# Kernel tuning notes

Measured on AMD Instinct MI355X. Metric: run time of the kernel, lower is better.

Reference implementation:

```python
import jax, jax.numpy as jnp
import numpy as np

N_HEAD, D_MODEL, D_K, D_V = 8, 512, 64, 64
B, LQ, LK = 32, 512, 512
NEG = -1e10
EPS = 1e-5


def setup_inputs() -> dict:
    key = jax.random.key(0)
    ks = jax.random.split(key, 9)
    q = jax.random.normal(ks[0], (B, LQ, D_MODEL), jnp.float32)
    k = jax.random.normal(ks[1], (B, LK, D_MODEL), jnp.float32)
    v = jax.random.normal(ks[2], (B, LK, D_MODEL), jnp.float32)
    mask = jax.random.randint(ks[3], (B, LQ, LK), 0, 2).astype(bool)
    std_qk = np.sqrt(2.0 / (D_MODEL + D_K)).astype(np.float32)
    std_v = np.sqrt(2.0 / (D_MODEL + D_V)).astype(np.float32)
    Wq = jax.random.normal(ks[4], (N_HEAD * D_K, D_MODEL), jnp.float32) * std_qk
    Wk = jax.random.normal(ks[5], (N_HEAD * D_K, D_MODEL), jnp.float32) * std_qk
    Wv = jax.random.normal(ks[6], (N_HEAD * D_V, D_MODEL), jnp.float32) * std_v
    fc_w = jax.random.normal(ks[7], (D_MODEL, N_HEAD * D_V), jnp.float32) * np.sqrt(2.0 / (D_MODEL + N_HEAD * D_V)).astype(np.float32)
    fc_b = jnp.zeros((D_MODEL,), jnp.float32)
    ln_g = jnp.ones((D_MODEL,), jnp.float32)
    ln_b = jnp.zeros((D_MODEL,), jnp.float32)
    return {"q": q, "k": k, "v": v, "mask": mask, "Wq": Wq, "Wk": Wk,
            "Wv": Wv, "fc_w": fc_w, "fc_b": fc_b, "ln_g": ln_g, "ln_b": ln_b}


def reference(q, k, v, mask, Wq, Wk, Wv, fc_w, fc_b, ln_g, ln_b):
    b, lq, _ = q.shape
    lk = k.shape[1]
    # projections (torch Linear: x @ W.T), reshape to [b, h, len, d]
    qh = (q @ Wq.T).reshape(b, lq, N_HEAD, D_K).transpose(0, 2, 1, 3)
    kh = (k @ Wk.T).reshape(b, lk, N_HEAD, D_K).transpose(0, 2, 1, 3)
    vh = (v @ Wv.T).reshape(b, lk, N_HEAD, D_V).transpose(0, 2, 1, 3)
    temperature = jnp.asarray(np.power(D_K, 0.5), qh.dtype)
    scores = jnp.einsum('bhqd,bhkd->bhqk', qh, kh) / temperature
    scores = jnp.where(mask[:, None, :, :], NEG, scores)  # masked_fill
    attn = jax.nn.softmax(scores, axis=-1)  # dropout in eval mode = identity
    out = jnp.einsum('bhqk,bhkd->bhqd', attn, vh)  # [b, h, lq, dv]
    out = out.transpose(0, 2, 1, 3).reshape(b, lq, N_HEAD * D_V)
    out = out @ fc_w.T + fc_b
    # layernorm over last dim
    mu = out.mean(-1, keepdims=True)
    var = ((out - mu) ** 2).mean(-1, keepdims=True)
    out = (out - mu) * jax.lax.rsqrt(var + EPS) * ln_g + ln_b
    # attn returned as [n_head*b, lq, lk] (head-major, matching torch view)
    attn_flat = attn.transpose(1, 0, 2, 3).reshape(N_HEAD * b, lq, lk)
    return out, attn_flat
```

## Files before the change

kernel.cpp:

```cpp
#include <hip/hip_runtime.h>
#include <stdint.h>


typedef float f32x4 __attribute__((ext_vector_type(4)));
typedef __bf16 bf16x8 __attribute__((ext_vector_type(8)));

#define DEV __device__ __forceinline__

DEV uint16_t f2bf(float f) {
  uint32_t u = __builtin_bit_cast(uint32_t, f);
  u += 0x7fffu + ((u >> 16) & 1u);
  return (uint16_t)(u >> 16);
}

DEV void gload_lds16(const void* g, void* l) {
  __builtin_amdgcn_global_load_lds((const __attribute__((address_space(1))) uint32_t*)g,
                                   (__attribute__((address_space(3))) uint32_t*)l, 16, 0, 0);
}

__global__ __launch_bounds__(256) void cvt_bf16(const float* __restrict__ src,
                                                uint16_t* __restrict__ dst, int n4) {
  int i = blockIdx.x * 256 + threadIdx.x;
  if (i >= n4) return;
  f32x4 v = ((const f32x4*)src)[i];
  ushort4 o;
  o.x = f2bf(v.x); o.y = f2bf(v.y); o.z = f2bf(v.z); o.w = f2bf(v.w);
  ((ushort4*)dst)[i] = o;
}

__global__ __launch_bounds__(256) void pack_mask(const int* __restrict__ m,
                                                 unsigned long long* __restrict__ pm, int nw) {
  int t = blockIdx.x * 256 + threadIdx.x;
  int wid = t >> 6, lane = t & 63;
  if (wid >= nw) return;
  int v = m[(size_t)wid * 64 + lane];
  unsigned long long bits = __ballot(v != 0);
  if (lane == 0) pm[wid] = bits;
}

template <int EPI>
__global__ __launch_bounds__(256) void gemm_nt(const uint16_t* __restrict__ A,
                                               const uint16_t* __restrict__ Bw,
                                               void* __restrict__ outp) {
  __shared__ uint16_t As[2][128 * 64];
  __shared__ uint16_t Bs[2][128 * 64];
  const int t = threadIdx.x;
  const int lane = t & 63;
  const int w = t >> 6;
  const int bn = blockIdx.x & 3;
  const int bm = blockIdx.x >> 2;
  const char* Ab = (const char*)(A + (size_t)bm * 128 * 512);
  const char* Bb = (const char*)(Bw + (size_t)bn * 128 * 512);
  const int l15 = lane & 15, l4 = lane >> 4;
  const int wr = (w >> 1) * 64, wc = (w & 1) * 64;

  auto stage = [&](int buf, int kt) {
    const int kb = kt * 128;
#pragma unroll
    for (int i = 0; i < 4; ++i) {
      int o = i * 4096 + t * 16;
      int row = o >> 7, cb = o & 127;
      int sw = cb ^ ((row & 7) << 4);
      gload_lds16(Ab + (size_t)row * 1024 + kb + sw, (char*)As[buf] + i * 4096 + (t & 192) * 16);
      gload_lds16(Bb + (size_t)row * 1024 + kb + sw, (char*)Bs[buf] + i * 4096 + (t & 192) * 16);
    }
  };

  f32x4 acc[4][4] = {};
  stage(0, 0);
  __syncthreads();
#pragma unroll 1
  for (int kt = 0; kt < 8; ++kt) {
    int cur = kt & 1;
    if (kt < 7) stage(cur ^ 1, kt + 1);
#pragma unroll
    for (int kk = 0; kk < 2; ++kk) {
      bf16x8 af[4], bf[4];
#pragma unroll
      for (int i = 0; i < 4; ++i) {
        int ar = wr + i * 16 + l15;
        af[i] = *(const bf16x8*)((const char*)As[cur] + ar * 128 +
                                 ((kk * 64 + l4 * 16) ^ ((ar & 7) << 4)));
        int br = wc + i * 16 + l15;
        bf[i] = *(const bf16x8*)((const char*)Bs[cur] + br * 128 +
                                 ((kk * 64 + l4 * 16) ^ ((br & 7) << 4)));
      }
#pragma unroll
      for (int i = 0; i < 4; ++i)
#pragma unroll
        for (int j = 0; j < 4; ++j)
          acc[i][j] = __builtin_amdgcn_mfma_f32_16x16x32_bf16(af[i], bf[j], acc[i][j], 0, 0, 0);
    }
    __syncthreads();
  }

  const int m0 = bm * 128 + wr + l4 * 4;
  const int n0 = bn * 128 + wc + l15;
#pragma unroll
  for (int i = 0; i < 4; ++i) {
#pragma unroll
    for (int j = 0; j < 4; ++j) {
      int mm = m0 + i * 16;
      int nn = n0 + j * 16;
      if (EPI == 2) {
        float* dst = (float*)outp + (size_t)mm * 512 + nn;
#pragma unroll
        for (int r = 0; r < 4; ++r) dst[(size_t)r * 512] = acc[i][j][r];
      } else {
        int b = mm >> 9, l = mm & 511;
        int h = nn >> 6, d = nn & 63;
        if (EPI == 0) {
          uint16_t* dst = (uint16_t*)outp + ((size_t)(b * 8 + h) * 512 + l) * 64 + d;
#pragma unroll
          for (int r = 0; r < 4; ++r) dst[(size_t)r * 64] = f2bf(acc[i][j][r]);
        } else {
          uint16_t* dst = (uint16_t*)outp + ((size_t)(b * 8 + h) * 64 + d) * 512 + l;
          ushort4 o;
          o.x = f2bf(acc[i][j][0]); o.y = f2bf(acc[i][j][1]);
          o.z = f2bf(acc[i][j][2]); o.w = f2bf(acc[i][j][3]);
          *(ushort4*)dst = o;
        }
      }
    }
  }
}

__global__ __launch_bounds__(512) void attn_fused(const uint16_t* __restrict__ qh,
                                                  const uint16_t* __restrict__ kh,
                                                  const uint16_t* __restrict__ vtp,
                                                  const unsigned long long* __restrict__ pm,
                                                  float* __restrict__ attn_out,
                                                  uint16_t* __restrict__ oh) {
  __shared__ uint16_t Qs[64 * 64];
  __shared__ uint16_t Ks[256 * 64];
  __shared__ uint16_t VTs[64 * 256];
  __shared__ uint16_t Ps[64 * 512];
  __shared__ float red8[64 * 8];
  __shared__ float redF[64];
  __shared__ float redS[64];

  const int bid = blockIdx.x;
  const int qb = bid & 7, h = (bid >> 3) & 7, b = bid >> 6;
  const int t = threadIdx.x, lane = t & 63, w = t >> 6;
  const int l15 = lane & 15, l4 = lane >> 4;
  const int q0 = qb * 64;
  const char* qbase = (const char*)(qh + ((size_t)(b * 8 + h) * 512 + q0) * 64);
  const char* kbase = (const char*)(kh + (size_t)(b * 8 + h) * 512 * 64);
  const char* vbase = (const char*)(vtp + (size_t)(b * 8 + h) * 64 * 512);

  auto stageK = [&](int p) {
#pragma unroll
    for (int i = 0; i < 4; ++i) {
      int o = i * 8192 + t * 16, row = o >> 7, cb = o & 127;
      gload_lds16(kbase + (size_t)(p * 256 + row) * 128 + (cb ^ ((row & 7) << 4)),
                  (char*)Ks + i * 8192 + (t & 448) * 16);
    }
  };
  auto stageV = [&](int p) {
#pragma unroll
    for (int i = 0; i < 4; ++i) {
      int o = i * 8192 + t * 16, row = o >> 9, cb = o & 511;
      gload_lds16(vbase + (size_t)row * 1024 + p * 512 + (cb ^ ((row & 7) << 4)),
                  (char*)VTs + i * 8192 + (t & 448) * 16);
    }
  };
  {
    int o = t * 16, row = o >> 7, cb = o & 127;
    gload_lds16(qbase + (size_t)row * 128 + (cb ^ ((row & 7) << 4)), (char*)Qs + (t & 448) * 16);
  }
  stageK(0);
  stageV(0);
  __syncthreads();

  bf16x8 af[4][2];
#pragma unroll
  for (int fq = 0; fq < 4; ++fq)
#pragma unroll
    for (int kk = 0; kk < 2; ++kk) {
      int ar = fq * 16 + l15;
      af[fq][kk] = *(const bf16x8*)((const char*)Qs + ar * 128 +
                                    ((kk * 64 + l4 * 16) ^ ((ar & 7) << 4)));
    }

  f32x4 sacc[4][4] = {};
#pragma unroll
  for (int fc = 0; fc < 2; ++fc) {
    int brow = w * 32 + fc * 16 + l15;
    bf16x8 b0 = *(const bf16x8*)((const char*)Ks + brow * 128 + ((l4 * 16) ^ ((brow & 7) << 4)));
    bf16x8 b1 = *(const bf16x8*)((const char*)Ks + brow * 128 + ((64 + l4 * 16) ^ ((brow & 7) << 4)));
#pragma unroll
    for (int fq = 0; fq < 4; ++fq) {
      sacc[fq][fc] = __builtin_amdgcn_mfma_f32_16x16x32_bf16(af[fq][0], b0, sacc[fq][fc], 0, 0, 0);
      sacc[fq][fc] = __builtin_amdgcn_mfma_f32_16x16x32_bf16(af[fq][1], b1, sacc[fq][fc], 0, 0, 0);
    }
  }
  __syncthreads();
  stageK(1);
  __syncthreads();
#pragma unroll
  for (int fc = 0; fc < 2; ++fc) {
    int brow = w * 32 + fc * 16 + l15;
    bf16x8 b0 = *(const bf16x8*)((const char*)Ks + brow * 128 + ((l4 * 16) ^ ((brow & 7) << 4)));
    bf16x8 b1 = *(const bf16x8*)((const char*)Ks + brow * 128 + ((64 + l4 * 16) ^ ((brow & 7) << 4)));
#pragma unroll
    for (int fq = 0; fq < 4; ++fq) {
      sacc[fq][2 + fc] = __builtin_amdgcn_mfma_f32_16x16x32_bf16(af[fq][0], b0, sacc[fq][2 + fc], 0, 0, 0);
      sacc[fq][2 + fc] = __builtin_amdgcn_mfma_f32_16x16x32_bf16(af[fq][1], b1, sacc[fq][2 + fc], 0, 0, 0);
    }
  }

  const size_t pmbase = ((size_t)b * 512 + q0) * 8;
#pragma unroll
  for (int fq = 0; fq < 4; ++fq) {
#pragma unroll
    for (int i = 0; i < 4; ++i) {
      int r = fq * 16 + l4 * 4 + i;
      unsigned long long m0 = pm[pmbase + r * 8 + (w >> 1)];
      unsigned long long m1 = pm[pmbase + r * 8 + 4 + (w >> 1)];
      int bit0 = (w & 1) * 32 + l15;
      float vmax = -3.0e38f;
#pragma unroll
      for (int fc = 0; fc < 4; ++fc) {
        unsigned long long word = (fc < 2) ? m0 : m1;
        int bit = bit0 + (fc & 1) * 16;
        bool mk = (word >> bit) & 1ull;
        float sv = sacc[fq][fc][i] * 0.125f;
        sv = mk ? -1.0e30f : sv;
        sacc[fq][fc][i] = sv;
        vmax = fmaxf(vmax, sv);
      }
      vmax = fmaxf(vmax, __shfl_xor(vmax, 1));
      vmax = fmaxf(vmax, __shfl_xor(vmax, 2));
      vmax = fmaxf(vmax, __shfl_xor(vmax, 4));
      vmax = fmaxf(vmax, __shfl_xor(vmax, 8));
      if (l15 == 0) red8[r * 8 + w] = vmax;
    }
  }
  __syncthreads();
  if (t < 64) {
    float m = red8[t * 8];
#pragma unroll
    for (int j = 1; j < 8; ++j) m = fmaxf(m, red8[t * 8 + j]);
    redF[t] = m;
  }
  __syncthreads();
#pragma unroll
  for (int fq = 0; fq < 4; ++fq) {
#pragma unroll
    for (int i = 0; i < 4; ++i) {
      int r = fq * 16 + l4 * 4 + i;
      float mx = redF[r];
      float s = 0.f;
#pragma unroll
      for (int fc = 0; fc < 4; ++fc) {
        float sv = sacc[fq][fc][i];
        float p = (sv < -1.0e29f) ? 0.f : __expf(sv - mx);
        sacc[fq][fc][i] = p;
        s += p;
      }
      s += __shfl_xor(s, 1); s += __shfl_xor(s, 2);
      s += __shfl_xor(s, 4); s += __shfl_xor(s, 8);
      if (l15 == 0) red8[r * 8 + w] = s;
    }
  }
  __syncthreads();
  if (t < 64) {
    float s = 0.f;
#pragma unroll
    for (int j = 0; j < 8; ++j) s += red8[t * 8 + j];
    redS[t] = 1.0f / s;
  }
  __syncthreads();

  float* abase = attn_out + ((size_t)(h * 32 + b) * 512 + q0) * 512;
#pragma unroll
  for (int fq = 0; fq < 4; ++fq) {
#pragma unroll
    for (int i = 0; i < 4; ++i) {
      int r = fq * 16 + l4 * 4 + i;
      float rinv = redS[r];
#pragma unroll
      for (int fc = 0; fc < 4; ++fc) {
        int c = ((fc >= 2) ? 256 : 0) + w * 32 + (fc & 1) * 16 + l15;
        float p = sacc[fq][fc][i] * rinv;
        abase[(size_t)r * 512 + c] = p;
        *(uint16_t*)((char*)Ps + r * 1024 + ((c * 2) ^ ((r & 7) << 4))) = f2bf(p);
      }
    }
  }
  __syncthreads();

  const int dfrag = w & 3, qsel = w >> 2;
  f32x4 oacc[2] = {};
  auto pvphase = [&](int p) {
#pragma unroll
    for (int ks = 0; ks < 8; ++ks) {
      int brow = dfrag * 16 + l15;
      bf16x8 bf = *(const bf16x8*)((const char*)VTs + brow * 512 +
                                   ((ks * 64 + l4 * 16) ^ ((brow & 7) << 4)));
#pragma unroll
      for (int qi = 0; qi < 2; ++qi) {
        int arow = (qsel * 2 + qi) * 16 + l15;
        int kb = (p * 256 + ks * 32 + l4 * 8) * 2;
        bf16x8 ap = *(const bf16x8*)((const char*)Ps + arow * 1024 + (kb ^ ((arow & 7) << 4)));
        oacc[qi] = __builtin_amdgcn_mfma_f32_16x16x32_bf16(ap, bf, oacc[qi], 0, 0, 0);
      }
    }
  };
  pvphase(0);
  __syncthreads();
  stageV(1);
  __syncthreads();
  pvphase(1);

#pragma unroll
  for (int qi = 0; qi < 2; ++qi) {
    int qrow = (qsel * 2 + qi) * 16 + l4 * 4;
    int d = dfrag * 16 + l15;
    uint16_t* dst = oh + ((size_t)(b * 512 + q0 + qrow)) * 512 + h * 64 + d;
#pragma unroll
    for (int r = 0; r < 4; ++r) dst[(size_t)r * 512] = f2bf(oacc[qi][r]);
  }
}

__global__ __launch_bounds__(256) void ln_kernel(const float* __restrict__ x,
                                                 const float* __restrict__ bias,
                                                 const float* __restrict__ g,
                                                 const float* __restrict__ bt,
                                                 float* __restrict__ out) {
  int w = threadIdx.x >> 6, lane = threadIdx.x & 63;
  int row = blockIdx.x * 4 + w;
  const float* xr = x + (size_t)row * 512;
  float v[8];
  float s = 0.f;
#pragma unroll
  for (int j = 0; j < 8; ++j) {
    v[j] = xr[lane + j * 64] + bias[lane + j * 64];
    s += v[j];
  }
#pragma unroll
  for (int m = 32; m >= 1; m >>= 1) s += __shfl_xor(s, m);
  float mu = s * (1.f / 512.f);
  float var = 0.f;
#pragma unroll
  for (int j = 0; j < 8; ++j) { float d = v[j] - mu; var += d * d; }
#pragma unroll
  for (int m = 32; m >= 1; m >>= 1) var += __shfl_xor(var, m);
  float rstd = rsqrtf(var * (1.f / 512.f) + 1e-5f);
  float* orow = out + (size_t)row * 512;
#pragma unroll
  for (int j = 0; j < 8; ++j)
    orow[lane + j * 64] = (v[j] - mu) * rstd * g[lane + j * 64] + bt[lane + j * 64];
}

extern "C" void kernel_launch(void* const* d_in, const int* in_sizes, int n_in,
                              void* d_out, int out_size, void* d_ws, size_t ws_size,
                              hipStream_t stream) {
  (void)in_sizes; (void)n_in; (void)out_size; (void)ws_size;
  const float* q   = (const float*)d_in[0];
  const float* k   = (const float*)d_in[1];
  const float* v   = (const float*)d_in[2];
  const int*   msk = (const int*)d_in[3];
  const float* Wq  = (const float*)d_in[4];
  const float* Wk  = (const float*)d_in[5];
  const float* Wv  = (const float*)d_in[6];
  const float* fcw = (const float*)d_in[7];
  const float* fcb = (const float*)d_in[8];
  const float* lng = (const float*)d_in[9];
  const float* lnb = (const float*)d_in[10];
  float* outp = (float*)d_out;

  char* ws = (char*)d_ws;
  uint16_t* qb_  = (uint16_t*)(ws);
  uint16_t* kb_  = (uint16_t*)(ws + 16777216);
  uint16_t* vb_  = (uint16_t*)(ws + 2 * 16777216);
  uint16_t* wqb  = (uint16_t*)(ws + 3 * 16777216);
  uint16_t* wkb  = (uint16_t*)(ws + 3 * 16777216 + 524288);
  uint16_t* wvb  = (uint16_t*)(ws + 3 * 16777216 + 2 * 524288);
  uint16_t* fcwb = (uint16_t*)(ws + 3 * 16777216 + 3 * 524288);
  uint16_t* qh   = (uint16_t*)(ws + 3 * 16777216 + 4 * 524288);
  uint16_t* kh   = qh + 8388608;
  uint16_t* vt   = kh + 8388608;
  uint16_t* oh   = vt + 8388608;
  float*    fco  = (float*)(oh + 8388608);
  unsigned long long* pmask = (unsigned long long*)((char*)fco + 33554432);

  cvt_bf16<<<8192, 256, 0, stream>>>(q, qb_, 2097152);
  cvt_bf16<<<8192, 256, 0, stream>>>(k, kb_, 2097152);
  cvt_bf16<<<8192, 256, 0, stream>>>(v, vb_, 2097152);
  cvt_bf16<<<256, 256, 0, stream>>>(Wq, wqb, 65536);
  cvt_bf16<<<256, 256, 0, stream>>>(Wk, wkb, 65536);
  cvt_bf16<<<256, 256, 0, stream>>>(Wv, wvb, 65536);
  cvt_bf16<<<256, 256, 0, stream>>>(fcw, fcwb, 65536);
  pack_mask<<<32768, 256, 0, stream>>>(msk, pmask, 131072);

  gemm_nt<0><<<512, 256, 0, stream>>>(qb_, wqb, qh);
  gemm_nt<0><<<512, 256, 0, stream>>>(kb_, wkb, kh);
  gemm_nt<1><<<512, 256, 0, stream>>>(vb_, wvb, vt);

  attn_fused<<<2048, 512, 0, stream>>>(qh, kh, vt, pmask, outp + 8388608, oh);

  gemm_nt<2><<<512, 256, 0, stream>>>(oh, fcwb, fco);
  ln_kernel<<<4096, 256, 0, stream>>>(fco, fcb, lng, lnb, outp);
}
```

Baseline: 620.6 us.

## Merge launches, read K/V directly in attention, coalesce attention-probability stores

Merges the seven conversion launches into two and the three projection GEMMs into one launch. Adds a tile remap to the GEMM block index, aimed at better L2 reuse. The attention kernel stops staging K and V through LDS and reads MFMA operands straight from global memory. It also drops the separate row-reduction barriers and raises wave priority around the MFMA loops. The fp32 attention matrix is now written as wide contiguous stores read back from the bf16 P tile in LDS. That removes scattered stores but means the returned attention probabilities are bf16-rounded, which risks failing accuracy tolerances.

```diff
diff --git a/kernel.cpp b/kernel.cpp
--- a/kernel.cpp
+++ b/kernel.cpp
@@ -4,6 +4,7 @@
 
 typedef float f32x4 __attribute__((ext_vector_type(4)));
 typedef __bf16 bf16x8 __attribute__((ext_vector_type(8)));
+typedef unsigned short ushort8 __attribute__((ext_vector_type(8)));
 
 #define DEV __device__ __forceinline__
 
@@ -18,14 +19,38 @@
                                    (__attribute__((address_space(3))) uint32_t*)l, 16, 0, 0);
 }
 
-__global__ __launch_bounds__(256) void cvt_bf16(const float* __restrict__ src,
-                                                uint16_t* __restrict__ dst, int n4) {
-  int i = blockIdx.x * 256 + threadIdx.x;
-  if (i >= n4) return;
-  f32x4 v = ((const f32x4*)src)[i];
+__global__ __launch_bounds__(256) void cvt_qkv(const float* __restrict__ q,
+                                               const float* __restrict__ k,
+                                               const float* __restrict__ v,
+                                               uint16_t* __restrict__ qo,
+                                               uint16_t* __restrict__ ko,
+                                               uint16_t* __restrict__ vo) {
+  int g = blockIdx.x >> 13;
+  int i = (blockIdx.x & 8191) * 256 + threadIdx.x;
+  const float* s = g == 0 ? q : g == 1 ? k : v;
+  uint16_t* d = g == 0 ? qo : g == 1 ? ko : vo;
+  f32x4 val = ((const f32x4*)s)[i];
   ushort4 o;
-  o.x = f2bf(v.x); o.y = f2bf(v.y); o.z = f2bf(v.z); o.w = f2bf(v.w);
-  ((ushort4*)dst)[i] = o;
+  o.x = f2bf(val.x); o.y = f2bf(val.y); o.z = f2bf(val.z); o.w = f2bf(val.w);
+  ((ushort4*)d)[i] = o;
+}
+
+__global__ __launch_bounds__(256) void cvt_w(const float* __restrict__ w0,
+                                             const float* __restrict__ w1,
+                                             const float* __restrict__ w2,
+                                             const float* __restrict__ w3,
+                                             uint16_t* __restrict__ d0,
+                                             uint16_t* __restrict__ d1,
+                                             uint16_t* __restrict__ d2,
+                                             uint16_t* __restrict__ d3) {
+  int g = blockIdx.x >> 8;
+  int i = (blockIdx.x & 255) * 256 + threadIdx.x;
+  const float* s = g == 0 ? w0 : g == 1 ? w1 : g == 2 ? w2 : w3;
+  uint16_t* d = g == 0 ? d0 : g == 1 ? d1 : g == 2 ? d2 : d3;
+  f32x4 val = ((const f32x4*)s)[i];
+  ushort4 o;
+  o.x = f2bf(val.x); o.y = f2bf(val.y); o.z = f2bf(val.z); o.w = f2bf(val.w);
+  ((ushort4*)d)[i] = o;
 }
 
 __global__ __launch_bounds__(256) void pack_mask(const int* __restrict__ m,
@@ -38,61 +63,73 @@
   if (lane == 0) pm[wid] = bits;
 }
 
-template <int EPI>
-__global__ __launch_bounds__(256) void gemm_nt(const uint16_t* __restrict__ A,
-                                               const uint16_t* __restrict__ Bw,
-                                               void* __restrict__ outp) {
+#define GEMM_CORE(Ab, Bb, As, Bs, acc)                                          \
+  {                                                                             \
+    auto stage = [&](int buf, int kt) {                                         \
+      const int kb = kt * 128;                                                  \
+      _Pragma("unroll") for (int i_ = 0; i_ < 4; ++i_) {                        \
+        int o_ = i_ * 4096 + t * 16;                                            \
+        int row_ = o_ >> 7, cb_ = o_ & 127;                                     \
+        int sw_ = cb_ ^ ((row_ & 7) << 4);                                      \
+        gload_lds16(Ab + (size_t)row_ * 1024 + kb + sw_,                        \
+                    (char*)As[buf] + i_ * 4096 + (t & 192) * 16);               \
+        gload_lds16(Bb + (size_t)row_ * 1024 + kb + sw_,                        \
+                    (char*)Bs[buf] + i_ * 4096 + (t & 192) * 16);               \
+      }                                                                         \
+    };                                                                          \
+    stage(0, 0);                                                                \
+    __syncthreads();                                                            \
+    _Pragma("unroll 1") for (int kt = 0; kt < 8; ++kt) {                        \
+      int cur = kt & 1;                                                         \
+      if (kt < 7) stage(cur ^ 1, kt + 1);                                       \
+      _Pragma("unroll") for (int kk = 0; kk < 2; ++kk) {                        \
+        bf16x8 af_[4], bf_[4];                                                  \
+        _Pragma("unroll") for (int i_ = 0; i_ < 4; ++i_) {                      \
+          int ar_ = wr + i_ * 16 + l15;                                         \
+          af_[i_] = *(const bf16x8*)((const char*)As[cur] + ar_ * 128 +         \
+                                     ((kk * 64 + l4 * 16) ^ ((ar_ & 7) << 4))); \
+          int br_ = wc + i_ * 16 + l15;                                         \
+          bf_[i_] = *(const bf16x8*)((const char*)Bs[cur] + br_ * 128 +         \
+                                     ((kk * 64 + l4 * 16) ^ ((br_ & 7) << 4))); \
+        }                                                                       \
+        _Pragma("unroll") for (int i_ = 0; i_ < 4; ++i_)                        \
+            _Pragma("unroll") for (int j_ = 0; j_ < 4; ++j_)                    \
+                acc[i_][j_] = __builtin_amdgcn_mfma_f32_16x16x32_bf16(          \
+                    af_[i_], bf_[j_], acc[i_][j_], 0, 0, 0);                    \
+      }                                                                         \
+      __syncthreads();                                                          \
+    }                                                                           \
+  }
+
+#define GEMM_BLOCKMAP()                        \
+  const int local = blockIdx.x & 511;          \
+  const int bm = (local & 7) * 16 + ((local >> 3) >> 2); \
+  const int bn = (local >> 3) & 3;             \
+  const int t = threadIdx.x;                   \
+  const int lane = t & 63;                     \
+  const int w = t >> 6;                        \
+  const int l15 = lane & 15, l4 = lane >> 4;   \
+  const int wr = (w >> 1) * 64, wc = (w & 1) * 64;
+
+__global__ __launch_bounds__(256) void gemm_proj(const uint16_t* __restrict__ qb,
+                                                 const uint16_t* __restrict__ kb,
+                                                 const uint16_t* __restrict__ vb,
+                                                 const uint16_t* __restrict__ wq,
+                                                 const uint16_t* __restrict__ wk,
+                                                 const uint16_t* __restrict__ wv,
+                                                 uint16_t* __restrict__ qh,
+                                                 uint16_t* __restrict__ kh,
+                                                 uint16_t* __restrict__ vt) {
   __shared__ uint16_t As[2][128 * 64];
   __shared__ uint16_t Bs[2][128 * 64];
-  const int t = threadIdx.x;
-  const int lane = t & 63;
-  const int w = t >> 6;
-  const int bn = blockIdx.x & 3;
-  const int bm = blockIdx.x >> 2;
+  const int g = blockIdx.x >> 9;
+  GEMM_BLOCKMAP();
+  const uint16_t* A = g == 0 ? qb : g == 1 ? kb : vb;
+  const uint16_t* W = g == 0 ? wq : g == 1 ? wk : wv;
   const char* Ab = (const char*)(A + (size_t)bm * 128 * 512);
-  const char* Bb = (const char*)(Bw + (size_t)bn * 128 * 512);
-  const int l15 = lane & 15, l4 = lane >> 4;
-  const int wr = (w >> 1) * 64, wc = (w & 1) * 64;
-
-  auto stage = [&](int buf, int kt) {
-    const int kb = kt * 128;
-#pragma unroll
-    for (int i = 0; i < 4; ++i) {
-      int o = i * 4096 + t * 16;
-      int row = o >> 7, cb = o & 127;
-      int sw = cb ^ ((row & 7) << 4);
-      gload_lds16(Ab + (size_t)row * 1024 + kb + sw, (char*)As[buf] + i * 4096 + (t & 192) * 16);
-      gload_lds16(Bb + (size_t)row * 1024 + kb + sw, (char*)Bs[buf] + i * 4096 + (t & 192) * 16);
-    }
-  };
-
+  const char* Bb = (const char*)(W + (size_t)bn * 128 * 512);
   f32x4 acc[4][4] = {};
-  stage(0, 0);
-  __syncthreads();
-#pragma unroll 1
-  for (int kt = 0; kt < 8; ++kt) {
-    int cur = kt & 1;
-    if (kt < 7) stage(cur ^ 1, kt + 1);
-#pragma unroll
-    for (int kk = 0; kk < 2; ++kk) {
-      bf16x8 af[4], bf[4];
-#pragma unroll
-      for (int i = 0; i < 4; ++i) {
-        int ar = wr + i * 16 + l15;
-        af[i] = *(const bf16x8*)((const char*)As[cur] + ar * 128 +
-                                 ((kk * 64 + l4 * 16) ^ ((ar & 7) << 4)));
-        int br = wc + i * 16 + l15;
-        bf[i] = *(const bf16x8*)((const char*)Bs[cur] + br * 128 +
-                                 ((kk * 64 + l4 * 16) ^ ((br & 7) << 4)));
-      }
-#pragma unroll
-      for (int i = 0; i < 4; ++i)
-#pragma unroll
-        for (int j = 0; j < 4; ++j)
-          acc[i][j] = __builtin_amdgcn_mfma_f32_16x16x32_bf16(af[i], bf[j], acc[i][j], 0, 0, 0);
-    }
-    __syncthreads();
-  }
+  GEMM_CORE(Ab, Bb, As, Bs, acc);
 
   const int m0 = bm * 128 + wr + l4 * 4;
   const int n0 = bn * 128 + wc + l15;
@@ -100,114 +137,88 @@
   for (int i = 0; i < 4; ++i) {
 #pragma unroll
     for (int j = 0; j < 4; ++j) {
-      int mm = m0 + i * 16;
-      int nn = n0 + j * 16;
-      if (EPI == 2) {
-        float* dst = (float*)outp + (size_t)mm * 512 + nn;
-#pragma unroll
-        for (int r = 0; r < 4; ++r) dst[(size_t)r * 512] = acc[i][j][r];
+      int mm = m0 + i * 16, nn = n0 + j * 16;
+      int b = mm >> 9, l = mm & 511;
+      int h = nn >> 6, d = nn & 63;
+      if (g < 2) {
+        uint16_t* dst = (g == 0 ? qh : kh) + ((size_t)(b * 8 + h) * 512 + l) * 64 + d;
+#pragma unroll
+        for (int r = 0; r < 4; ++r) dst[(size_t)r * 64] = f2bf(acc[i][j][r]);
       } else {
-        int b = mm >> 9, l = mm & 511;
-        int h = nn >> 6, d = nn & 63;
-        if (EPI == 0) {
-          uint16_t* dst = (uint16_t*)outp + ((size_t)(b * 8 + h) * 512 + l) * 64 + d;
-#pragma unroll
-          for (int r = 0; r < 4; ++r) dst[(size_t)r * 64] = f2bf(acc[i][j][r]);
-        } else {
-          uint16_t* dst = (uint16_t*)outp + ((size_t)(b * 8 + h) * 64 + d) * 512 + l;
-          ushort4 o;
-          o.x = f2bf(acc[i][j][0]); o.y = f2bf(acc[i][j][1]);
-          o.z = f2bf(acc[i][j][2]); o.w = f2bf(acc[i][j][3]);
-          *(ushort4*)dst = o;
-        }
+        uint16_t* dst = vt + ((size_t)(b * 8 + h) * 64 + d) * 512 + l;
+        ushort4 o;
+        o.x = f2bf(acc[i][j][0]); o.y = f2bf(acc[i][j][1]);
+        o.z = f2bf(acc[i][j][2]); o.w = f2bf(acc[i][j][3]);
+        *(ushort4*)dst = o;
       }
     }
   }
 }
 
-__global__ __launch_bounds__(512) void attn_fused(const uint16_t* __restrict__ qh,
-                                                  const uint16_t* __restrict__ kh,
-                                                  const uint16_t* __restrict__ vtp,
-                                                  const unsigned long long* __restrict__ pm,
-                                                  float* __restrict__ attn_out,
-                                                  uint16_t* __restrict__ oh) {
-  __shared__ uint16_t Qs[64 * 64];
-  __shared__ uint16_t Ks[256 * 64];
-  __shared__ uint16_t VTs[64 * 256];
+__global__ __launch_bounds__(256) void gemm_fc(const uint16_t* __restrict__ A,
+                                               const uint16_t* __restrict__ W,
+                                               float* __restrict__ fco) {
+  __shared__ uint16_t As[2][128 * 64];
+  __shared__ uint16_t Bs[2][128 * 64];
+  GEMM_BLOCKMAP();
+  const char* Ab = (const char*)(A + (size_t)bm * 128 * 512);
+  const char* Bb = (const char*)(W + (size_t)bn * 128 * 512);
+  f32x4 acc[4][4] = {};
+  GEMM_CORE(Ab, Bb, As, Bs, acc);
+
+  const int m0 = bm * 128 + wr + l4 * 4;
+  const int n0 = bn * 128 + wc + l15;
+#pragma unroll
+  for (int i = 0; i < 4; ++i)
+#pragma unroll
+    for (int j = 0; j < 4; ++j) {
+      float* dst = fco + (size_t)(m0 + i * 16) * 512 + n0 + j * 16;
+#pragma unroll
+      for (int r = 0; r < 4; ++r) dst[(size_t)r * 512] = acc[i][j][r];
+    }
+}
+
+__global__ __launch_bounds__(512, 4) void attn_fused(const uint16_t* __restrict__ qh,
+                                                     const uint16_t* __restrict__ kh,
+                                                     const uint16_t* __restrict__ vtp,
+                                                     const unsigned long long* __restrict__ pm,
+                                                     float* __restrict__ attn_out,
+                                                     uint16_t* __restrict__ oh) {
   __shared__ uint16_t Ps[64 * 512];
-  __shared__ float red8[64 * 8];
-  __shared__ float redF[64];
-  __shared__ float redS[64];
+  __shared__ float red8[64 * 9];
+  __shared__ float red8b[64 * 9];
 
   const int bid = blockIdx.x;
-  const int qb = bid & 7, h = (bid >> 3) & 7, b = bid >> 6;
+  const int bh = bid & 255, qb = bid >> 8;
+  const int b = bh >> 3, h = bh & 7;
   const int t = threadIdx.x, lane = t & 63, w = t >> 6;
   const int l15 = lane & 15, l4 = lane >> 4;
   const int q0 = qb * 64;
-  const char* qbase = (const char*)(qh + ((size_t)(b * 8 + h) * 512 + q0) * 64);
-  const char* kbase = (const char*)(kh + (size_t)(b * 8 + h) * 512 * 64);
-  const char* vbase = (const char*)(vtp + (size_t)(b * 8 + h) * 64 * 512);
-
-  auto stageK = [&](int p) {
-#pragma unroll
-    for (int i = 0; i < 4; ++i) {
-      int o = i * 8192 + t * 16, row = o >> 7, cb = o & 127;
-      gload_lds16(kbase + (size_t)(p * 256 + row) * 128 + (cb ^ ((row & 7) << 4)),
-                  (char*)Ks + i * 8192 + (t & 448) * 16);
-    }
-  };
-  auto stageV = [&](int p) {
-#pragma unroll
-    for (int i = 0; i < 4; ++i) {
-      int o = i * 8192 + t * 16, row = o >> 9, cb = o & 511;
-      gload_lds16(vbase + (size_t)row * 1024 + p * 512 + (cb ^ ((row & 7) << 4)),
-                  (char*)VTs + i * 8192 + (t & 448) * 16);
-    }
-  };
-  {
-    int o = t * 16, row = o >> 7, cb = o & 127;
-    gload_lds16(qbase + (size_t)row * 128 + (cb ^ ((row & 7) << 4)), (char*)Qs + (t & 448) * 16);
-  }
-  stageK(0);
-  stageV(0);
-  __syncthreads();
+  const char* qbase = (const char*)qh + ((size_t)bh * 512 + q0) * 128;
+  const char* kbase = (const char*)kh + (size_t)bh * 512 * 128;
+  const char* vbase = (const char*)vtp + (size_t)bh * 64 * 1024;
 
   bf16x8 af[4][2];
 #pragma unroll
   for (int fq = 0; fq < 4; ++fq)
 #pragma unroll
-    for (int kk = 0; kk < 2; ++kk) {
-      int ar = fq * 16 + l15;
-      af[fq][kk] = *(const bf16x8*)((const char*)Qs + ar * 128 +
-                                    ((kk * 64 + l4 * 16) ^ ((ar & 7) << 4)));
-    }
+    for (int kk = 0; kk < 2; ++kk)
+      af[fq][kk] = *(const bf16x8*)(qbase + (fq * 16 + l15) * 128 + kk * 64 + l4 * 16);
 
   f32x4 sacc[4][4] = {};
-#pragma unroll
-  for (int fc = 0; fc < 2; ++fc) {
-    int brow = w * 32 + fc * 16 + l15;
-    bf16x8 b0 = *(const bf16x8*)((const char*)Ks + brow * 128 + ((l4 * 16) ^ ((brow & 7) << 4)));
-    bf16x8 b1 = *(const bf16x8*)((const char*)Ks + brow * 128 + ((64 + l4 * 16) ^ ((brow & 7) << 4)));
+  __builtin_amdgcn_s_setprio(1);
+#pragma unroll
+  for (int fc = 0; fc < 4; ++fc) {
+    int brow = (fc >> 1) * 256 + w * 32 + (fc & 1) * 16 + l15;
+    bf16x8 b0 = *(const bf16x8*)(kbase + (size_t)brow * 128 + l4 * 16);
+    bf16x8 b1 = *(const bf16x8*)(kbase + (size_t)brow * 128 + 64 + l4 * 16);
 #pragma unroll
     for (int fq = 0; fq < 4; ++fq) {
       sacc[fq][fc] = __builtin_amdgcn_mfma_f32_16x16x32_bf16(af[fq][0], b0, sacc[fq][fc], 0, 0, 0);
       sacc[fq][fc] = __builtin_amdgcn_mfma_f32_16x16x32_bf16(af[fq][1], b1, sacc[fq][fc], 0, 0, 0);
     }
   }
-  __syncthreads();
-  stageK(1);
-  __syncthreads();
-#pragma unroll
-  for (int fc = 0; fc < 2; ++fc) {
-    int brow = w * 32 + fc * 16 + l15;
-    bf16x8 b0 = *(const bf16x8*)((const char*)Ks + brow * 128 + ((l4 * 16) ^ ((brow & 7) << 4)));
-    bf16x8 b1 = *(const bf16x8*)((const char*)Ks + brow * 128 + ((64 + l4 * 16) ^ ((brow & 7) << 4)));
-#pragma unroll
-    for (int fq = 0; fq < 4; ++fq) {
-      sacc[fq][2 + fc] = __builtin_amdgcn_mfma_f32_16x16x32_bf16(af[fq][0], b0, sacc[fq][2 + fc], 0, 0, 0);
-      sacc[fq][2 + fc] = __builtin_amdgcn_mfma_f32_16x16x32_bf16(af[fq][1], b1, sacc[fq][2 + fc], 0, 0, 0);
-    }
-  }
+  __builtin_amdgcn_s_setprio(0);
 
   const size_t pmbase = ((size_t)b * 512 + q0) * 8;
 #pragma unroll
@@ -222,8 +233,7 @@
 #pragma unroll
       for (int fc = 0; fc < 4; ++fc) {
         unsigned long long word = (fc < 2) ? m0 : m1;
-        int bit = bit0 + (fc & 1) * 16;
-        bool mk = (word >> bit) & 1ull;
+        bool mk = (word >> (bit0 + (fc & 1) * 16)) & 1ull;
         float sv = sacc[fq][fc][i] * 0.125f;
         sv = mk ? -1.0e30f : sv;
         sacc[fq][fc][i] = sv;
@@ -233,85 +243,87 @@
       vmax = fmaxf(vmax, __shfl_xor(vmax, 2));
       vmax = fmaxf(vmax, __shfl_xor(vmax, 4));
       vmax = fmaxf(vmax, __shfl_xor(vmax, 8));
-      if (l15 == 0) red8[r * 8 + w] = vmax;
+      if (l15 == 0) red8[r * 9 + w] = vmax;
     }
   }
   __syncthreads();
-  if (t < 64) {
-    float m = red8[t * 8];
-#pragma unroll
-    for (int j = 1; j < 8; ++j) m = fmaxf(m, red8[t * 8 + j]);
-    redF[t] = m;
-  }
-  __syncthreads();
+
 #pragma unroll
   for (int fq = 0; fq < 4; ++fq) {
 #pragma unroll
     for (int i = 0; i < 4; ++i) {
       int r = fq * 16 + l4 * 4 + i;
-      float mx = redF[r];
+      float mx = red8[r * 9];
+#pragma unroll
+      for (int j = 1; j < 8; ++j) mx = fmaxf(mx, red8[r * 9 + j]);
       float s = 0.f;
 #pragma unroll
       for (int fc = 0; fc < 4; ++fc) {
-        float sv = sacc[fq][fc][i];
-        float p = (sv < -1.0e29f) ? 0.f : __expf(sv - mx);
+        float p = __expf(sacc[fq][fc][i] - mx);
         sacc[fq][fc][i] = p;
         s += p;
       }
       s += __shfl_xor(s, 1); s += __shfl_xor(s, 2);
       s += __shfl_xor(s, 4); s += __shfl_xor(s, 8);
-      if (l15 == 0) red8[r * 8 + w] = s;
+      if (l15 == 0) red8b[r * 9 + w] = s;
     }
   }
   __syncthreads();
-  if (t < 64) {
-    float s = 0.f;
-#pragma unroll
-    for (int j = 0; j < 8; ++j) s += red8[t * 8 + j];
-    redS[t] = 1.0f / s;
-  }
-  __syncthreads();
-
-  float* abase = attn_out + ((size_t)(h * 32 + b) * 512 + q0) * 512;
+
 #pragma unroll
   for (int fq = 0; fq < 4; ++fq) {
 #pragma unroll
     for (int i = 0; i < 4; ++i) {
       int r = fq * 16 + l4 * 4 + i;
-      float rinv = redS[r];
+      float s = red8b[r * 9];
+#pragma unroll
+      for (int j = 1; j < 8; ++j) s += red8b[r * 9 + j];
+      float rinv = 1.0f / s;
 #pragma unroll
       for (int fc = 0; fc < 4; ++fc) {
-        int c = ((fc >= 2) ? 256 : 0) + w * 32 + (fc & 1) * 16 + l15;
-        float p = sacc[fq][fc][i] * rinv;
-        abase[(size_t)r * 512 + c] = p;
-        *(uint16_t*)((char*)Ps + r * 1024 + ((c * 2) ^ ((r & 7) << 4))) = f2bf(p);
+        int c = (fc >> 1) * 256 + w * 32 + (fc & 1) * 16 + l15;
+        *(uint16_t*)((char*)Ps + r * 1024 + ((c * 2) ^ ((r & 7) << 4))) =
+            f2bf(sacc[fq][fc][i] * rinv);
       }
     }
   }
   __syncthreads();
+
+  {
+    float* abase = attn_out + ((size_t)(h * 32 + b) * 512 + q0) * 512;
+    int r = t >> 3, s8 = t & 7;
+#pragma unroll
+    for (int j = 0; j < 8; ++j) {
+      bf16x8 pv = *(const bf16x8*)((const char*)Ps + r * 1024 +
+                                   ((j * 128 + s8 * 16) ^ ((r & 7) << 4)));
+      ushort8 u = __builtin_bit_cast(ushort8, pv);
+      f32x4 lo, hi;
+#pragma unroll
+      for (int c = 0; c < 4; ++c) {
+        lo[c] = __builtin_bit_cast(float, (uint32_t)u[c] << 16);
+        hi[c] = __builtin_bit_cast(float, (uint32_t)u[c + 4] << 16);
+      }
+      char* dst = (char*)abase + (size_t)r * 2048 + j * 256 + s8 * 32;
+      *(f32x4*)dst = lo;
+      *(f32x4*)(dst + 16) = hi;
+    }
+  }
 
   const int dfrag = w & 3, qsel = w >> 2;
   f32x4 oacc[2] = {};
-  auto pvphase = [&](int p) {
-#pragma unroll
-    for (int ks = 0; ks < 8; ++ks) {
-      int brow = dfrag * 16 + l15;
-      bf16x8 bf = *(const bf16x8*)((const char*)VTs + brow * 512 +
-                                   ((ks * 64 + l4 * 16) ^ ((brow & 7) << 4)));
-#pragma unroll
-      for (int qi = 0; qi < 2; ++qi) {
-        int arow = (qsel * 2 + qi) * 16 + l15;
-        int kb = (p * 256 + ks * 32 + l4 * 8) * 2;
-        bf16x8 ap = *(const bf16x8*)((const char*)Ps + arow * 1024 + (kb ^ ((arow & 7) << 4)));
-        oacc[qi] = __builtin_amdgcn_mfma_f32_16x16x32_bf16(ap, bf, oacc[qi], 0, 0, 0);
-      }
-    }
-  };
-  pvphase(0);
-  __syncthreads();
-  stageV(1);
-  __syncthreads();
-  pvphase(1);
+  __builtin_amdgcn_s_setprio(1);
+#pragma unroll
+  for (int kc = 0; kc < 16; ++kc) {
+    bf16x8 bv = *(const bf16x8*)(vbase + (size_t)(dfrag * 16 + l15) * 1024 + kc * 64 + l4 * 16);
+#pragma unroll
+    for (int qi = 0; qi < 2; ++qi) {
+      int arow = (qsel * 2 + qi) * 16 + l15;
+      bf16x8 ap = *(const bf16x8*)((const char*)Ps + arow * 1024 +
+                                   ((kc * 64 + l4 * 16) ^ ((arow & 7) << 4)));
+      oacc[qi] = __builtin_amdgcn_mfma_f32_16x16x32_bf16(ap, bv, oacc[qi], 0, 0, 0);
+    }
+  }
+  __builtin_amdgcn_s_setprio(0);
 
 #pragma unroll
   for (int qi = 0; qi < 2; ++qi) {
@@ -385,21 +397,14 @@
   float*    fco  = (float*)(oh + 8388608);
   unsigned long long* pmask = (unsigned long long*)((char*)fco + 33554432);
 
-  cvt_bf16<<<8192, 256, 0, stream>>>(q, qb_, 2097152);
-  cvt_bf16<<<8192, 256, 0, stream>>>(k, kb_, 2097152);
-  cvt_bf16<<<8192, 256, 0, stream>>>(v, vb_, 2097152);
-  cvt_bf16<<<256, 256, 0, stream>>>(Wq, wqb, 65536);
-  cvt_bf16<<<256, 256, 0, stream>>>(Wk, wkb, 65536);
-  cvt_bf16<<<256, 256, 0, stream>>>(Wv, wvb, 65536);
-  cvt_bf16<<<256, 256, 0, stream>>>(fcw, fcwb, 65536);
+  cvt_qkv<<<24576, 256, 0, stream>>>(q, k, v, qb_, kb_, vb_);
+  cvt_w<<<1024, 256, 0, stream>>>(Wq, Wk, Wv, fcw, wqb, wkb, wvb, fcwb);
   pack_mask<<<32768, 256, 0, stream>>>(msk, pmask, 131072);
 
-  gemm_nt<0><<<512, 256, 0, stream>>>(qb_, wqb, qh);
-  gemm_nt<0><<<512, 256, 0, stream>>>(kb_, wkb, kh);
-  gemm_nt<1><<<512, 256, 0, stream>>>(vb_, wvb, vt);
+  gemm_proj<<<1536, 256, 0, stream>>>(qb_, kb_, vb_, wqb, wkb, wvb, qh, kh, vt);
 
   attn_fused<<<2048, 512, 0, stream>>>(qh, kh, vt, pmask, outp + 8388608, oh);
 
-  gemm_nt<2><<<512, 256, 0, stream>>>(oh, fcwb, fco);
+  gemm_fc<<<512, 256, 0, stream>>>(oh, fcwb, fco);
   ln_kernel<<<4096, 256, 0, stream>>>(fco, fcb, lng, lnb, outp);
 }
```

Measured after the change: 601.3 us. 3.1% less time.
